# Kernel tuning notes

Hardware: AMD Instinct MI355X
Metric: run time of the kernel (lower is better)

The kernel has to match this reference:

```python
import jax, jax.numpy as jnp
import numpy as np

IMG_DIM = 512
BATCH = 32


def setup_inputs() -> dict:
    key = jax.random.key(0)
    k1, k2, k3, k4, k5 = jax.random.split(key, 5)
    N, D = BATCH, IMG_DIM
    return {
        "im1": jax.random.normal(k1, (N, 3, D, D), jnp.float32),
        "im2": jax.random.normal(k2, (N, 3, D, D), jnp.float32),
        "C": jax.random.normal(k3, (N, 2, D, D), jnp.float32),
        "M1": jax.random.uniform(k4, (N, 1, D, D), jnp.float32),
        "M2": jax.random.uniform(k5, (N, 1, D, D), jnp.float32),
    }


def _grid_q(D):
    # q[0] = row coord repeated, q[1] = col coord tiled -> [2, D*D]
    x = jnp.arange(D, dtype=jnp.float32)
    return jnp.stack([jnp.repeat(x, D), jnp.tile(x, D)], axis=0)


def _get_pixel(qi, nb_x, nb_y, imflat, D):
    # qi: [N,2,HW]; nb_x, nb_y: [N,HW] integer-valued floats; imflat: [N,3,HW]
    w = (1.0 - jnp.abs(qi[:, 0] - nb_x)) * (1.0 - jnp.abs(qi[:, 1] - nb_y))  # [N,HW]
    inds = (nb_y + D * nb_x).astype(jnp.int32)  # ind = y + D*x, detached from grads
    inds = jax.lax.stop_gradient(inds)
    px = jnp.take_along_axis(imflat, inds[:, None, :], axis=2)  # [N,3,HW]
    return w[:, None, :] * px


def _masked_rp(image, mask, qi_orig, D):
    N = image.shape[0]
    HW = D * D
    imflat = image.reshape(N, 3, HW)
    qi = jnp.clip(qi_orig, 0.001, D - 1.001)  # [N,2,HW]
    fx, fy = jnp.floor(qi[:, 0]), jnp.floor(qi[:, 1])
    cx, cy = jnp.ceil(qi[:, 0]), jnp.ceil(qi[:, 1])
    res = (_get_pixel(qi, fx, fy, imflat, D)
           + _get_pixel(qi, cx, fy, imflat, D)
           + _get_pixel(qi, fx, cy, imflat, D)
           + _get_pixel(qi, cx, cy, imflat, D))  # [N,3,HW]
    oob_loss = jnp.mean((qi_orig - qi) ** 2) / (D * D) * 0.01
    res_img = res.reshape(image.shape)
    return res_img * mask, oob_loss


def _forward(im1, im2, C, M1, M2):
    N = im1.shape[0]
    D = im1.shape[2]
    q = _grid_q(D)[None]  # [1,2,HW]
    Cflat = C.reshape(N, 2, D * D)
    a, la = _masked_rp(im1, M1, q + Cflat, D)
    b, lb = _masked_rp(im2, M2, q - Cflat, D)
    return a + b, la + lb


def reference(im1, im2, C, M1, M2):
    return _forward(im1, im2, C, M1, M2)
```

## Files before the change

kernel.cpp:

```cpp
#include <hip/hip_runtime.h>


constexpr int D    = 512;
constexpr int HW   = D * D;
constexpr int NB   = 32;
constexpr int NPIX = NB * HW;
constexpr float LOSS_SCALE = (float)(0.01 / (2.0 * (double)NPIX * (double)HW));

typedef float f4 __attribute__((ext_vector_type(4)));

constexpr int WROWS   = 10;
constexpr int RSTRIDE = 512;
constexpr int PLANE   = WROWS * RSTRIDE;
constexpr int LDSZ    = 2 * PLANE;
constexpr int INLIM   = (WROWS - 1) << 9;

__device__ __forceinline__ float lerp2(float v00, float v01, float v10, float v11,
                                       float ax, float ay)
{
    float top = fmaf(ay, v01 - v00, v00);
    float bot = fmaf(ay, v11 - v10, v10);
    return fmaf(ax, bot - top, top);
}

__global__ void __launch_bounds__(256)
__attribute__((amdgpu_waves_per_eu(4, 4)))
vm_fwd(const float* __restrict__ im1, const float* __restrict__ im2,
       const float* __restrict__ C,   const float* __restrict__ M1,
       const float* __restrict__ M2,  float* __restrict__ out)
{
    __shared__ float lds[LDSZ];

    const int b    = blockIdx.x;
    const int slab = ((b & 7) << 10) | (b >> 3);

    const int n   = slab >> 8;
    const int k   = slab & 255;
    const int r   = k << 1;
    const int tid = threadIdx.x;
    const int hw0 = (k << 10) | tid;
    const int wlo = min(max(r - 4, 0), D - WROWS);
    const int wbase = wlo << 9;

    const float* Cn = C   + (size_t)n * 2 * HW;
    const float* Mp = M1  + (size_t)n * HW;
    const float* Mq = M2  + (size_t)n * HW;
    const float* p1 = im1 + (size_t)n * 3 * HW;
    const float* p2 = im2 + (size_t)n * 3 * HW;
    float* op       = out + (size_t)n * 3 * HW;

    const int su  = (tid >> 7);
    const int sc4 = (tid & 127) << 2;

    f4 pf[10];
    #define PFLOAD(CH)                                                          \
        _Pragma("unroll")                                                       \
        for (int q = 0; q < 10; ++q) {                                          \
            const float* ip = (q < 5) ? p1 : p2;                                \
            int u = (q % 5) * 2 + su;                                           \
            pf[q] = *(const f4*)(ip + (size_t)(CH) * HW + ((wlo + u) << 9) + sc4); \
        }
    #define PFWRITE()                                                           \
        _Pragma("unroll")                                                       \
        for (int q = 0; q < 10; ++q) {                                          \
            int u = (q % 5) * 2 + su;                                           \
            int img = (q < 5) ? 0 : 1;                                          \
            *(f4*)(lds + img * PLANE + u * RSTRIDE + sc4) = pf[q];              \
        }

    PFLOAD(0);

    float oob = 0.0f;
    float axA[4], ayA[4], w1v[4], axB[4], ayB[4], w2v[4];
    int   offA[4], offB[4];

    #pragma unroll
    for (int j = 0; j < 4; ++j) {
        const int hw = hw0 + j * 256;
        const float qx = (float)(hw >> 9);
        const float qy = (float)(hw & 511);
        float c0 = __builtin_nontemporal_load(Cn + hw);
        float c1 = __builtin_nontemporal_load(Cn + HW + hw);
        float m1 = __builtin_nontemporal_load(Mp + hw);
        float m2 = __builtin_nontemporal_load(Mq + hw);

        const float hi = 510.999f;
        {
            float q0o = qx + c0, q1o = qy + c1;
            float q0 = fminf(fmaxf(q0o, 0.001f), hi);
            float q1 = fminf(fmaxf(q1o, 0.001f), hi);
            float d0 = q0o - q0, d1 = q1o - q1;
            oob = fmaf(d0, d0, oob); oob = fmaf(d1, d1, oob);
            float fx = floorf(q0), fy = floorf(q1);
            axA[j] = q0 - fx; ayA[j] = q1 - fy;
            float sc = ((axA[j] == 0.0f) ? 2.0f : 1.0f) * ((ayA[j] == 0.0f) ? 2.0f : 1.0f);
            w1v[j] = m1 * sc;
            offA[j] = (int)fy + (((int)fx) << 9);
        }
        {
            float q0o = qx - c0, q1o = qy - c1;
            float q0 = fminf(fmaxf(q0o, 0.001f), hi);
            float q1 = fminf(fmaxf(q1o, 0.001f), hi);
            float d0 = q0o - q0, d1 = q1o - q1;
            oob = fmaf(d0, d0, oob); oob = fmaf(d1, d1, oob);
            float fx = floorf(q0), fy = floorf(q1);
            axB[j] = q0 - fx; ayB[j] = q1 - fy;
            float sc = ((axB[j] == 0.0f) ? 2.0f : 1.0f) * ((ayB[j] == 0.0f) ? 2.0f : 1.0f);
            w2v[j] = m2 * sc;
            offB[j] = (int)fy + (((int)fx) << 9);
        }
    }

    #pragma unroll
    for (int ch = 0; ch < 3; ++ch) {
        PFWRITE();
        __syncthreads();
        if (ch < 2) PFLOAD(ch + 1);

        const float* g1 = p1 + (size_t)ch * HW;
        const float* g2 = p2 + (size_t)ch * HW;
        float* oc = op + (size_t)ch * HW;

        #pragma unroll
        for (int j = 0; j < 4; ++j) {
            float ra, rb;
            int relA = offA[j] - wbase;
            if ((unsigned)relA < (unsigned)INLIM) {
                float2 t0, t1;
                __builtin_memcpy(&t0, &lds[relA], 8);
                __builtin_memcpy(&t1, &lds[relA + RSTRIDE], 8);
                ra = lerp2(t0.x, t0.y, t1.x, t1.y, axA[j], ayA[j]);
            } else {
                const float* pa = g1 + offA[j];
                ra = lerp2(pa[0], pa[1], pa[512], pa[513], axA[j], ayA[j]);
            }
            int relB = offB[j] - wbase;
            if ((unsigned)relB < (unsigned)INLIM) {
                float2 t0, t1;
                __builtin_memcpy(&t0, &lds[PLANE + relB], 8);
                __builtin_memcpy(&t1, &lds[PLANE + relB + RSTRIDE], 8);
                rb = lerp2(t0.x, t0.y, t1.x, t1.y, axB[j], ayB[j]);
            } else {
                const float* pb = g2 + offB[j];
                rb = lerp2(pb[0], pb[1], pb[512], pb[513], axB[j], ayB[j]);
            }
            __builtin_nontemporal_store(fmaf(ra, w1v[j], rb * w2v[j]),
                                        oc + hw0 + j * 256);
        }
        __syncthreads();
    }

    #pragma unroll
    for (int off = 32; off > 0; off >>= 1)
        oob += __shfl_down(oob, off, 64);

    int lane = tid & 63;
    int wave = tid >> 6;
    if (lane == 0) lds[wave] = oob;
    __syncthreads();
    if (tid == 0) {
        float s = lds[0] + lds[1] + lds[2] + lds[3];
        atomicAdd(out + (size_t)3 * NPIX, s * LOSS_SCALE);
    }
}

extern "C" void kernel_launch(void* const* d_in, const int* in_sizes, int n_in,
                              void* d_out, int out_size, void* d_ws, size_t ws_size,
                              hipStream_t stream) {
    const float* im1 = (const float*)d_in[0];
    const float* im2 = (const float*)d_in[1];
    const float* C   = (const float*)d_in[2];
    const float* M1  = (const float*)d_in[3];
    const float* M2  = (const float*)d_in[4];
    float* out = (float*)d_out;

    hipMemsetAsync(out + (size_t)3 * NPIX, 0, sizeof(float), stream);

    vm_fwd<<<8192, 256, 0, stream>>>(im1, im2, C, M1, M2, out);
}
```

Baseline: 367.4 us.

## Stage image windows into LDS with direct global-to-LDS loads

Replaces the register-staged prefetch (global load into VGPRs, then LDS write) with direct global_load_lds 16-byte transfers into shared memory, and drops the fixed waves-per-EU attribute. The aim is to cut VGPR pressure and the extra LDS write instructions. In exchange, the next channel's load is now issued only after the current channel's compute, with a barrier right after it. This removes the overlap of prefetch with compute that the old code had.

```diff
diff --git a/kernel.cpp b/kernel.cpp
--- a/kernel.cpp
+++ b/kernel.cpp
@@ -6,8 +6,6 @@
 constexpr int NB   = 32;
 constexpr int NPIX = NB * HW;
 constexpr float LOSS_SCALE = (float)(0.01 / (2.0 * (double)NPIX * (double)HW));
-
-typedef float f4 __attribute__((ext_vector_type(4)));
 
 constexpr int WROWS   = 10;
 constexpr int RSTRIDE = 512;
@@ -23,8 +21,14 @@
     return fmaf(ax, bot - top, top);
 }
 
+__device__ __forceinline__ void gload_lds16(const float* g, float* l)
+{
+    __builtin_amdgcn_global_load_lds(
+        (const __attribute__((address_space(1))) void*)g,
+        (__attribute__((address_space(3))) void*)l, 16, 0, 0);
+}
+
 __global__ void __launch_bounds__(256)
-__attribute__((amdgpu_waves_per_eu(4, 4)))
 vm_fwd(const float* __restrict__ im1, const float* __restrict__ im2,
        const float* __restrict__ C,   const float* __restrict__ M1,
        const float* __restrict__ M2,  float* __restrict__ out)
@@ -49,26 +53,22 @@
     const float* p2 = im2 + (size_t)n * 3 * HW;
     float* op       = out + (size_t)n * 3 * HW;
 
-    const int su  = (tid >> 7);
-    const int sc4 = (tid & 127) << 2;
+    const int w    = tid >> 6;
+    const int lane = tid & 63;
+    const int half = (w & 1) << 8;
+    const int su   = w >> 1;
+    const int lf   = lane << 2;
 
-    f4 pf[10];
-    #define PFLOAD(CH)                                                          \
+    #define ISSUE(CH)                                                           \
         _Pragma("unroll")                                                       \
         for (int q = 0; q < 10; ++q) {                                          \
             const float* ip = (q < 5) ? p1 : p2;                                \
             int u = (q % 5) * 2 + su;                                           \
-            pf[q] = *(const f4*)(ip + (size_t)(CH) * HW + ((wlo + u) << 9) + sc4); \
-        }
-    #define PFWRITE()                                                           \
-        _Pragma("unroll")                                                       \
-        for (int q = 0; q < 10; ++q) {                                          \
-            int u = (q % 5) * 2 + su;                                           \
-            int img = (q < 5) ? 0 : 1;                                          \
-            *(f4*)(lds + img * PLANE + u * RSTRIDE + sc4) = pf[q];              \
+            gload_lds16(ip + (size_t)(CH) * HW + ((wlo + u) << 9) + half + lf,  \
+                        lds + ((q < 5) ? 0 : PLANE) + u * RSTRIDE + half + lf); \
         }
 
-    PFLOAD(0);
+    ISSUE(0);
 
     float oob = 0.0f;
     float axA[4], ayA[4], w1v[4], axB[4], ayB[4], w2v[4];
@@ -111,12 +111,10 @@
         }
     }
 
+    __syncthreads();
+
     #pragma unroll
     for (int ch = 0; ch < 3; ++ch) {
-        PFWRITE();
-        __syncthreads();
-        if (ch < 2) PFLOAD(ch + 1);
-
         const float* g1 = p1 + (size_t)ch * HW;
         const float* g2 = p2 + (size_t)ch * HW;
         float* oc = op + (size_t)ch * HW;
@@ -148,15 +146,17 @@
                                         oc + hw0 + j * 256);
         }
         __syncthreads();
+        if (ch < 2) {
+            ISSUE(ch + 1);
+            __syncthreads();
+        }
     }
 
     #pragma unroll
     for (int off = 32; off > 0; off >>= 1)
         oob += __shfl_down(oob, off, 64);
 
-    int lane = tid & 63;
-    int wave = tid >> 6;
-    if (lane == 0) lds[wave] = oob;
+    if (lane == 0) lds[w] = oob;
     __syncthreads();
     if (tid == 0) {
         float s = lds[0] + lds[1] + lds[2] + lds[3];
```

Measured after the change: 343.1 us. 1.07x faster.
